# Performance work log

Measured on AMD Instinct MI355X. Metric: run time of the kernel, lower is better.

Reference implementation:

```python
import jax, jax.numpy as jnp
import numpy as np

POOLED = 7      # pooled_size
KSIZE = 2       # kernel_size (max-pool window & stride)
CROP = POOLED * KSIZE  # crop_and_resize crop_size = 14


def setup_inputs() -> dict:
    key = jax.random.key(0)
    k1, k2 = jax.random.split(key)
    feature_maps = jax.random.normal(k1, (2, 50, 50, 512), dtype=jnp.float32)
    # normalized boxes in [x1, y1, x2, y2] order (the layer swaps to y1,x1,y2,x2);
    # tf.image.crop_and_resize handles arbitrary (even inverted) boxes, so raw
    # uniforms are valid inputs.
    rois = jax.random.uniform(k2, (2, 128, 4), dtype=jnp.float32)
    return {"feature_maps": feature_maps, "rois": rois}


def _roi_pool(feature_maps, rois):
    B, H, W, C = feature_maps.shape
    R = rois.shape[1]
    N = B * R
    # [x1,y1,x2,y2] -> [y1,x1,y2,x2] as in the layer
    boxes = rois.reshape(N, 4)[:, jnp.array([1, 0, 3, 2])]
    y1, x1, y2, x2 = boxes[:, 0], boxes[:, 1], boxes[:, 2], boxes[:, 3]
    bidx = jnp.repeat(jnp.arange(B), R)  # box_indices, [N]

    # tf.image.crop_and_resize sample grid (crop_size > 1 branch)
    i = jnp.arange(CROP, dtype=feature_maps.dtype)
    ys = y1[:, None] * (H - 1) + i[None, :] * ((y2 - y1)[:, None] * (H - 1) / (CROP - 1))  # [N,S]
    xs = x1[:, None] * (W - 1) + i[None, :] * ((x2 - x1)[:, None] * (W - 1) / (CROP - 1))  # [N,S]
    valid_y = (ys >= 0) & (ys <= H - 1)
    valid_x = (xs >= 0) & (xs <= W - 1)

    y0f = jnp.floor(ys)
    x0f = jnp.floor(xs)
    wy = (ys - y0f)[:, :, None, None]   # [N,S,1,1]
    wx = (xs - x0f)[:, None, :, None]   # [N,1,S,1]
    y0i = jnp.clip(y0f.astype(jnp.int32), 0, H - 1)
    y1i = jnp.clip(y0i + 1, 0, H - 1)
    x0i = jnp.clip(x0f.astype(jnp.int32), 0, W - 1)
    x1i = jnpp = None
    x1i = jnp.clip(x0i + 1, 0, W - 1)

    # gather the two bilinear rows per sample line: [N, S, W, C]
    rows0 = feature_maps[bidx[:, None], y0i]
    rows1 = feature_maps[bidx[:, None], y1i]
    rows = rows0 + (rows1 - rows0) * wy  # lerp in y

    # gather the two columns and lerp in x: [N, S, S, C]
    v0 = jnp.take_along_axis(rows, x0i[:, None, :, None], axis=2)
    v1 = jnp.take_along_axis(rows, x1i[:, None, :, None], axis=2)
    crops = v0 + (v1 - v0) * wx

    # out-of-range samples -> extrapolation_value = 0 (TF default)
    valid = valid_y[:, :, None, None] & valid_x[:, None, :, None]
    crops = jnp.where(valid, crops, jnp.zeros((), crops.dtype))

    # 2x2/stride-2 max pool -> [N, POOLED, POOLED, C]
    pooled = crops.reshape(N, POOLED, KSIZE, POOLED, KSIZE, C).max(axis=(2, 4))
    return pooled


def reference(feature_maps, rois):
    # flatten=False, keep_batch_dim=False -> [batch*num_rois, pooled, pooled, C]
    return _roi_pool(feature_maps, rois)
```

## Files before the change

kernel.cpp:

```cpp
#include <hip/hip_runtime.h>
#include <hip/hip_fp16.h>


constexpr int H = 50, W = 50, C = 512;
constexpr int POOLEDX = 7, KSIZE = 2, CROP = 14;
constexpr int RPB = 128;
constexpr int PIX = POOLEDX * POOLEDX;
constexpr int NROI = 2 * RPB;
constexpr int NTASK = NROI * PIX;
constexpr int NELEM = 2 * H * W * C;

typedef _Float16 h8 __attribute__((ext_vector_type(8)));

__global__ __launch_bounds__(256) void cvt_kernel(
    const float* __restrict__ in, __half* __restrict__ out)
{
    const int i = (blockIdx.x * 256 + threadIdx.x) * 8;
    const float4* in4 = reinterpret_cast<const float4*>(in + i);
    const float4 a = in4[0];
    const float4 b = in4[1];
    __half h[8];
    h[0]=__float2half(a.x); h[1]=__float2half(a.y); h[2]=__float2half(a.z); h[3]=__float2half(a.w);
    h[4]=__float2half(b.x); h[5]=__float2half(b.y); h[6]=__float2half(b.z); h[7]=__float2half(b.w);
    *reinterpret_cast<float4*>(out + i) = *reinterpret_cast<const float4*>(h);
}

__global__ __launch_bounds__(256, 4) void roi_pool_kernel(
    const __half* __restrict__ fmh,
    const float* __restrict__ rois,
    float* __restrict__ out)
{
    const int task = blockIdx.x * 4 + (threadIdx.x >> 6);
    const int lane = threadIdx.x & 63;
    const int n  = task / PIX;
    const int k  = task - n * PIX;
    const int ph = k / POOLEDX;
    const int pw = k - ph * POOLEDX;
    const int bat = n / RPB;

    const float rx1 = rois[n*4+0], ry1 = rois[n*4+1];
    const float rx2 = rois[n*4+2], ry2 = rois[n*4+3];
    const float ybase = ry1 * (float)(H - 1);
    const float xbase = rx1 * (float)(W - 1);
    const float ystep = ((ry2 - ry1) * (float)(H - 1)) / (float)(CROP - 1);
    const float xstep = ((rx2 - rx1) * (float)(W - 1)) / (float)(CROP - 1);

    int   x0i[KSIZE], x1i[KSIZE];
    float wx[KSIZE];
    bool  vx[KSIZE];
    #pragma unroll
    for (int kx = 0; kx < KSIZE; ++kx) {
        const float xs = xbase + (float)(pw * KSIZE + kx) * xstep;
        vx[kx] = (xs >= 0.0f) && (xs <= (float)(W - 1));
        const float xf = floorf(xs);
        wx[kx] = xs - xf;
        int xi = (int)xf; xi = min(max(xi, 0), W - 1);
        x0i[kx] = xi;
        x1i[kx] = min(xi + 1, W - 1);
    }

    const __half* base = fmh + (long)bat * (H * W) * C + lane * 8;

    h8 acc;
    #pragma unroll
    for (int c = 0; c < 8; ++c) acc[c] = (_Float16)(-60000.0f);

    #pragma unroll
    for (int ky = 0; ky < KSIZE; ++ky) {
        const float ys = ybase + (float)(ph * KSIZE + ky) * ystep;
        const bool  vy = (ys >= 0.0f) && (ys <= (float)(H - 1));
        const float yf = floorf(ys);
        const float wy = ys - yf;
        int y0 = (int)yf; y0 = min(max(y0, 0), H - 1);
        const int y1 = min(y0 + 1, H - 1);

        #pragma unroll
        for (int kx = 0; kx < KSIZE; ++kx) {
            const h8 t00 = *reinterpret_cast<const h8*>(base + (long)(y0 * W + x0i[kx]) * C);
            const h8 t01 = *reinterpret_cast<const h8*>(base + (long)(y0 * W + x1i[kx]) * C);
            const h8 t10 = *reinterpret_cast<const h8*>(base + (long)(y1 * W + x0i[kx]) * C);
            const h8 t11 = *reinterpret_cast<const h8*>(base + (long)(y1 * W + x1i[kx]) * C);

            const float wxk = wx[kx];
            const _Float16 w00 = (_Float16)((1.0f - wy) * (1.0f - wxk));
            const _Float16 w01 = (_Float16)((1.0f - wy) * wxk);
            const _Float16 w10 = (_Float16)(wy * (1.0f - wxk));
            const _Float16 w11 = (_Float16)(wy * wxk);

            h8 v = t00 * w00 + t01 * w01 + t10 * w10 + t11 * w11;

            if (!(vx[kx] && vy)) {
                #pragma unroll
                for (int c = 0; c < 8; ++c) v[c] = (_Float16)0.0f;
            }

#if __has_builtin(__builtin_elementwise_max)
            acc = __builtin_elementwise_max(acc, v);
#else
            #pragma unroll
            for (int c = 0; c < 8; ++c) acc[c] = acc[c] > v[c] ? acc[c] : v[c];
#endif
        }
    }

    float4 o0, o1;
    o0.x = (float)acc[0]; o0.y = (float)acc[1]; o0.z = (float)acc[2]; o0.w = (float)acc[3];
    o1.x = (float)acc[4]; o1.y = (float)acc[5]; o1.z = (float)acc[6]; o1.w = (float)acc[7];
    float4* out4 = reinterpret_cast<float4*>(out) + (long)task * (C / 4) + lane * 2;
    out4[0] = o0;
    out4[1] = o1;
}

extern "C" void kernel_launch(void* const* d_in, const int* in_sizes, int n_in,
                              void* d_out, int out_size, void* d_ws, size_t ws_size,
                              hipStream_t stream) {
    const float* fm   = (const float*)d_in[0];
    const float* rois = (const float*)d_in[1];
    float* out  = (float*)d_out;
    __half* fmh = (__half*)d_ws;

    cvt_kernel<<<NELEM / (256 * 8), 256, 0, stream>>>(fm, fmh);
    roi_pool_kernel<<<NTASK / 4, 256, 0, stream>>>(fmh, rois, out);
}
```

Measured before the change: 79.57 us.

## Swizzle ROI blocks across XCDs and use nontemporal loads/stores

Block IDs are remapped so that each of the 8 XCDs processes a contiguous chunk of tasks. ROIs sharing the same feature-map region then hit the same XCD's L2 instead of being scattered round-robin. The fp32 input read in the conversion kernel and the fp32 output stores use nontemporal hints to avoid polluting cache. The remap assumes blocks are dispatched round-robin across 8 XCDs and that NBLK is divisible by 8.

```diff
diff --git a/kernel.cpp b/kernel.cpp
--- a/kernel.cpp
+++ b/kernel.cpp
@@ -9,20 +9,26 @@
 constexpr int NROI = 2 * RPB;
 constexpr int NTASK = NROI * PIX;
 constexpr int NELEM = 2 * H * W * C;
+constexpr int NBLK  = NTASK / 4;
+constexpr int NXCD  = 8;
+constexpr int CHUNK = NBLK / NXCD;
 
 typedef _Float16 h8 __attribute__((ext_vector_type(8)));
+typedef float    f4 __attribute__((ext_vector_type(4)));
 
 __global__ __launch_bounds__(256) void cvt_kernel(
     const float* __restrict__ in, __half* __restrict__ out)
 {
     const int i = (blockIdx.x * 256 + threadIdx.x) * 8;
-    const float4* in4 = reinterpret_cast<const float4*>(in + i);
-    const float4 a = in4[0];
-    const float4 b = in4[1];
-    __half h[8];
-    h[0]=__float2half(a.x); h[1]=__float2half(a.y); h[2]=__float2half(a.z); h[3]=__float2half(a.w);
-    h[4]=__float2half(b.x); h[5]=__float2half(b.y); h[6]=__float2half(b.z); h[7]=__float2half(b.w);
-    *reinterpret_cast<float4*>(out + i) = *reinterpret_cast<const float4*>(h);
+    const f4* in4 = reinterpret_cast<const f4*>(in + i);
+    const f4 a = __builtin_nontemporal_load(in4);
+    const f4 b = __builtin_nontemporal_load(in4 + 1);
+    _Float16 h[8];
+    h[0] = (_Float16)a[0]; h[1] = (_Float16)a[1];
+    h[2] = (_Float16)a[2]; h[3] = (_Float16)a[3];
+    h[4] = (_Float16)b[0]; h[5] = (_Float16)b[1];
+    h[6] = (_Float16)b[2]; h[7] = (_Float16)b[3];
+    *reinterpret_cast<f4*>(out + i) = *reinterpret_cast<const f4*>(h);
 }
 
 __global__ __launch_bounds__(256, 4) void roi_pool_kernel(
@@ -30,8 +36,13 @@
     const float* __restrict__ rois,
     float* __restrict__ out)
 {
-    const int task = blockIdx.x * 4 + (threadIdx.x >> 6);
+    const int wv   = __builtin_amdgcn_readfirstlane((int)(threadIdx.x >> 6));
     const int lane = threadIdx.x & 63;
+
+    const int bid  = blockIdx.x;
+    const int swz  = (bid & (NXCD - 1)) * CHUNK + (bid >> 3);
+    const int task = swz * 4 + wv;
+
     const int n  = task / PIX;
     const int k  = task - n * PIX;
     const int ph = k / POOLEDX;
@@ -103,12 +114,12 @@
         }
     }
 
-    float4 o0, o1;
-    o0.x = (float)acc[0]; o0.y = (float)acc[1]; o0.z = (float)acc[2]; o0.w = (float)acc[3];
-    o1.x = (float)acc[4]; o1.y = (float)acc[5]; o1.z = (float)acc[6]; o1.w = (float)acc[7];
-    float4* out4 = reinterpret_cast<float4*>(out) + (long)task * (C / 4) + lane * 2;
-    out4[0] = o0;
-    out4[1] = o1;
+    f4 o0, o1;
+    o0[0] = (float)acc[0]; o0[1] = (float)acc[1]; o0[2] = (float)acc[2]; o0[3] = (float)acc[3];
+    o1[0] = (float)acc[4]; o1[1] = (float)acc[5]; o1[2] = (float)acc[6]; o1[3] = (float)acc[7];
+    f4* out4 = reinterpret_cast<f4*>(out) + (long)task * (C / 4) + lane * 2;
+    __builtin_nontemporal_store(o0, out4);
+    __builtin_nontemporal_store(o1, out4 + 1);
 }
 
 extern "C" void kernel_launch(void* const* d_in, const int* in_sizes, int n_in,
@@ -120,5 +131,5 @@
     __half* fmh = (__half*)d_ws;
 
     cvt_kernel<<<NELEM / (256 * 8), 256, 0, stream>>>(fm, fmh);
-    roi_pool_kernel<<<NTASK / 4, 256, 0, stream>>>(fmh, rois, out);
+    roi_pool_kernel<<<NBLK, 256, 0, stream>>>(fmh, rois, out);
 }
```

Result: no change. 78.83 us (-0.9%).
